# Performance work log

Hardware: AMD Instinct MI355X
Metric: run time of the kernel (lower is better)

## Reference

```python
import jax, jax.numpy as jnp
from jax import lax
import numpy as np

B, T, TW, EW = 32, 64, 32, 300   # dialogues, utterances, words, word-embed
H = 512                          # lstm hidden per direction
E = 2 * H                        # utterance embedding size
HH = 512                         # emotion hidden size
C = 7                            # output classes


def setup_inputs() -> dict:
    key = jax.random.key(0)
    ks = jax.random.split(key, 24)
    n = lambda k, shp: (jax.random.normal(k, shp, dtype=jnp.float32) * 0.05)
    inp = {
        "input_data": jax.random.normal(ks[0], (B, T, TW, EW), dtype=jnp.float32),
        # BiLSTM (torch gate order i,f,g,o)
        "lstm_Wih_f": n(ks[1], (4 * H, EW)), "lstm_Whh_f": n(ks[2], (4 * H, H)), "lstm_b_f": n(ks[3], (4 * H,)),
        "lstm_Wih_b": n(ks[4], (4 * H, EW)), "lstm_Whh_b": n(ks[5], (4 * H, H)), "lstm_b_b": n(ks[6], (4 * H,)),
        # attention weight
        "W_att": n(ks[7], (E, E)),
        # global-state GRUCell (torch gate order r,z,n)
        "g_Wih": n(ks[8], (3 * E, E)), "g_Whh": n(ks[9], (3 * E, E)), "g_bih": n(ks[10], (3 * E,)), "g_bhh": n(ks[11], (3 * E,)),
        # party-state GRUCell
        "p_Wih": n(ks[12], (3 * E, E)), "p_Whh": n(ks[13], (3 * E, E)), "p_bih": n(ks[14], (3 * E,)), "p_bhh": n(ks[15], (3 * E,)),
        # emotion-state GRUCell (input E, hidden HH)
        "e_Wih": n(ks[16], (3 * HH, E)), "e_Whh": n(ks[17], (3 * HH, HH)), "e_bih": n(ks[18], (3 * HH,)), "e_bhh": n(ks[19], (3 * HH,)),
        # classifier
        "cls_W": n(ks[20], (C, HH)), "cls_b": n(ks[21], (C,)),
    }
    return inp


def _gru_cell(x, h, Wih, Whh, bih, bhh):
    gi = x @ Wih.T + bih
    gh = h @ Whh.T + bhh
    ir, iz, inn = jnp.split(gi, 3, axis=-1)
    hr, hz, hn = jnp.split(gh, 3, axis=-1)
    r = jax.nn.sigmoid(ir + hr)
    z = jax.nn.sigmoid(iz + hz)
    n = jnp.tanh(inn + r * hn)
    return (1.0 - z) * n + z * h


def _lstm_last_hidden(xs, Wih, Whh, b):
    # xs: [Tw, N, Ew] -> final hidden [N, H]
    N = xs.shape[1]
    h0 = jnp.zeros((N, H), xs.dtype)

    def step(carry, x):
        h, c = carry
        g = x @ Wih.T + h @ Whh.T + b
        i_, f_, g_, o_ = jnp.split(g, 4, axis=-1)
        c2 = jax.nn.sigmoid(f_) * c + jax.nn.sigmoid(i_) * jnp.tanh(g_)
        h2 = jax.nn.sigmoid(o_) * jnp.tanh(c2)
        return (h2, c2), None

    (h, _), _ = lax.scan(step, (h0, h0), xs)
    return h


def _forward(input_data, lstm_Wih_f, lstm_Whh_f, lstm_b_f, lstm_Wih_b, lstm_Whh_b, lstm_b_b,
             W_att, g_Wih, g_Whh, g_bih, g_bhh, p_Wih, p_Whh, p_bih, p_bhh,
             e_Wih, e_Whh, e_bih, e_bhh, cls_W, cls_b):
    # ---- FeatureExtraction: BiLSTM over words, take fwd-last + bwd-first hidden ----
    x = input_data.reshape(B * T, TW, EW).transpose(1, 0, 2)          # [Tw, N, Ew]
    h_fwd = _lstm_last_hidden(x, lstm_Wih_f, lstm_Whh_f, lstm_b_f)     # [N, H]
    h_bwd = _lstm_last_hidden(x[::-1], lstm_Wih_b, lstm_Whh_b, lstm_b_b)  # [N, H]
    feats = jnp.concatenate([h_fwd, h_bwd], axis=-1).reshape(B, T, E)  # [B, T, 2H]

    # ---- EmotionDetection: sequential recurrence over utterances ----
    utt = feats.transpose(1, 0, 2)                                     # [T, B, E]
    hist0 = jnp.zeros((T + 1, B, E), feats.dtype)   # global_state history (idx 0 = zero init)
    party0 = jnp.zeros((2, B, E), feats.dtype)
    emo0 = jnp.zeros((B, HH), feats.dtype)
    l_idx = jnp.arange(T + 1)[:, None]              # [T+1, 1]

    def step(carry, inp):
        hist, party, emo = carry
        x_i, i = inp
        p = i % 2
        g_prev = hist[i]                                               # global_state[i]
        new_g = _gru_cell(x_i + party[p], g_prev, g_Wih, g_Whh, g_bih, g_bhh)
        hist = hist.at[i + 1].set(new_g)
        # attention over history indices 0..i (excludes the just-appended state)
        q = x_i @ W_att                                                # [B, E]
        scores = jnp.einsum('be,lbe->lb', q, hist)                     # [T+1, B]
        scores = jnp.where(l_idx <= i, scores, -jnp.inf)
        w = jax.nn.softmax(scores, axis=0)[:, :, None]                 # [T+1, B, 1]
        context = jnp.sum(hist * w, axis=0)                            # [B, E]
        new_p = _gru_cell(x_i + context, party[p], p_Wih, p_Whh, p_bih, p_bhh)
        party = party.at[p].set(new_p)
        emo = _gru_cell(new_p, emo, e_Wih, e_Whh, e_bih, e_bhh)        # [B, HH]
        return (hist, party, emo), emo

    _, emo_seq = lax.scan(step, (hist0, party0, emo0), (utt, jnp.arange(T)))
    emo_seq = emo_seq.transpose(1, 0, 2)                               # [B, T, HH]
    return emo_seq @ cls_W.T + cls_b                                   # [B, T, C]


def reference(input_data, lstm_Wih_f, lstm_Whh_f, lstm_b_f, lstm_Wih_b, lstm_Whh_b, lstm_b_b,
              W_att, g_Wih, g_Whh, g_bih, g_bhh, p_Wih, p_Whh, p_bih, p_bhh,
              e_Wih, e_Whh, e_bih, e_bhh, cls_W, cls_b):
    return _forward(input_data, lstm_Wih_f, lstm_Whh_f, lstm_b_f, lstm_Wih_b, lstm_Whh_b, lstm_b_b,
                    W_att, g_Wih, g_Whh, g_bih, g_bhh, p_Wih, p_Whh, p_bih, p_bhh,
                    e_Wih, e_Whh, e_bih, e_bhh, cls_W, cls_b)
```

## Files before the change

kernel.cpp:

```cpp
#include <hip/hip_runtime.h>
#include <math.h>

#define B_  32
#define T_  64
#define TW_ 32
#define EW_ 300
#define H_  512
#define E_  1024
#define HH_ 512
#define C_  7
#define N_  2048

typedef float f32x4 __attribute__((ext_vector_type(4)));
typedef short s16x8 __attribute__((ext_vector_type(8)));
typedef unsigned short u16;
typedef unsigned int u32;

__device__ __forceinline__ float sigm(float x){ return 1.f/(1.f+expf(-x)); }
__device__ __forceinline__ float bf2f(u16 u){
  union{float f; unsigned v;} x; x.v = ((unsigned)u)<<16; return x.f;
}
__device__ __forceinline__ u16 f2bf(float f){
  union{float f; unsigned v;} x; x.f = f;
  unsigned r = x.v + 0x7FFF + ((x.v>>16)&1);
  return (u16)(r>>16);
}
__device__ __forceinline__ void g2lds16(const void* g, void* l){
  __builtin_amdgcn_global_load_lds((const __attribute__((address_space(1))) u32*)g,
                                   (__attribute__((address_space(3))) u32*)l, 16, 0, 0);
}

__global__ __launch_bounds__(256) void k_pack_w(
    const float* __restrict__ Wih_f, const float* __restrict__ Whh_f,
    const float* __restrict__ Wih_b, const float* __restrict__ Whh_b,
    u16* __restrict__ Wpk2)
{
  size_t idx = (size_t)blockIdx.x*256 + threadIdx.x;
  if(idx >= (size_t)64*26*2048) return;
  int c   = (int)(idx & 31);
  int row = (int)((idx >> 5) & 63);
  int kc  = (int)((idx >> 11) % 26);
  int pan = (int)(idx / ((size_t)26*2048));
  int dir = pan >> 5, ms = pan & 31;
  int g = row >> 4, ml = row & 15;
  int R = g*512 + ms*16 + ml;
  int k = kc*32 + c;
  const float* Wih = dir ? Wih_b : Wih_f;
  const float* Whh = dir ? Whh_b : Whh_f;
  float v = (k < 320) ? ((k < EW_) ? Wih[(size_t)R*EW_ + k] : 0.f)
                      : Whh[(size_t)R*H_ + (k-320)];
  Wpk2[idx] = f2bf(v);
}

__global__ __launch_bounds__(256) void k_pack_x(
    const float* __restrict__ input, u16* __restrict__ xpk)
{
  size_t idx = (size_t)blockIdx.x*256 + threadIdx.x;
  if(idx >= (size_t)32*32*10*2048) return;
  int c   = (int)(idx & 31);
  int row = (int)((idx >> 5) & 63);
  int kc  = (int)((idx >> 11) % 10);
  int q2  = (int)((idx >> 11) / 10);
  int nt  = q2 & 31, wt = q2 >> 5;
  int n = nt*64 + row;
  int k = kc*32 + c;
  float v = (k < EW_) ? input[((size_t)n*TW_ + wt)*EW_ + k] : 0.f;
  xpk[idx] = f2bf(v);
}

__global__ __launch_bounds__(256) void k_f2bf(const float* __restrict__ src,
                                              u16* __restrict__ dst, int n)
{
  int idx = blockIdx.x*256 + threadIdx.x;
  if(idx < n) dst[idx] = f2bf(src[idx]);
}

__global__ __launch_bounds__(256) void k_wattT(const float* __restrict__ W,
                                               u16* __restrict__ dst)
{
  int idx = blockIdx.x*256 + threadIdx.x;
  if(idx >= E_*E_) return;
  int j = idx >> 10, k = idx & 1023;
  dst[idx] = f2bf(W[(size_t)k*E_ + j]);
}

__global__ __launch_bounds__(256, 6) void lstm6(
    const u16* __restrict__ xpk, const u16* __restrict__ Wpk2,
    const float* __restrict__ b_f, const float* __restrict__ b_b,
    const u16* __restrict__ hpk_in, u16* __restrict__ hpk_out,
    float* __restrict__ cpk, u16* __restrict__ featsbf, int t)
{
  const int pan = blockIdx.x, nt = blockIdx.y;
  const int dir = pan & 1, ms = pan >> 1;
  const int wt = dir ? (TW_-1-t) : t;
  const u16* srcW = Wpk2 + (size_t)(dir*32+ms)*26*2048;
  const u16* srcX = xpk + (size_t)(wt*32+nt)*10*2048;
  const u16* srcH = hpk_in + (size_t)(dir*32+nt)*16*2048;

  __shared__ __align__(16) u16 As[3][2048];
  __shared__ __align__(16) u16 Bs[3][2048];

  const int tid = threadIdx.x;
  const int w = tid >> 6, l = tid & 63;
  const int lr = l & 15, lh = l >> 4;

  f32x4 acc[4];
  #pragma unroll
  for(int g=0;g<4;g++) acc[g] = (f32x4){0.f,0.f,0.f,0.f};

  auto stage = [&](int kc, int b){
    const u16* aB = (kc < 10) ? (srcX + (size_t)kc*2048) : (srcH + (size_t)(kc-10)*2048);
    const u16* bB = srcW + (size_t)kc*2048;
    g2lds16((const char*)aB + w*1024 + l*16, (char*)&As[b][0] + w*1024);
    g2lds16((const char*)bB + w*1024 + l*16, (char*)&Bs[b][0] + w*1024);
  };

  stage(0, 0);
  stage(1, 1);
  #pragma unroll
  for(int kc=0; kc<26; ++kc){
    if(kc < 25) asm volatile("s_waitcnt vmcnt(2)" ::: "memory");
    else        asm volatile("s_waitcnt vmcnt(0)" ::: "memory");
    __builtin_amdgcn_s_barrier();
    __builtin_amdgcn_sched_barrier(0);
    if(kc+2 < 26) stage(kc+2, (kc+2)%3);
    const int cu = kc % 3;
    s16x8 av = *(const s16x8*)&As[cu][(w*16 + lr)*32 + lh*8];
    #pragma unroll
    for(int g=0; g<4; ++g){
      s16x8 bv = *(const s16x8*)&Bs[cu][(g*16 + lr)*32 + lh*8];
      acc[g] = __builtin_amdgcn_mfma_f32_16x16x32_bf16(av, bv, acc[g], 0,0,0);
    }
  }

  const float* bias = dir ? b_b : b_f;
  const int m = ms*16 + lr;
  const float bi = bias[m], bfv = bias[H_+m], bg = bias[2*H_+m], bo = bias[3*H_+m];
  float* cp = cpk + ((size_t)(dir*32+nt)*32 + ms)*1024;
  u16* hop = hpk_out + ((size_t)(dir*32+nt)*16 + (ms>>1))*2048 + (ms&1)*16;
  const int n0 = nt*64;
  #pragma unroll
  for(int r=0; r<4; ++r){
    const int row = w*16 + lh*4 + r;
    float gi = acc[0][r] + bi;
    float gf = acc[1][r] + bfv;
    float gc = acc[2][r] + bg;
    float go = acc[3][r] + bo;
    float c_old = cp[row*16 + lr];
    float c2 = sigm(gf)*c_old + sigm(gi)*tanhf(gc);
    float h2 = sigm(go)*tanhf(c2);
    cp[row*16 + lr] = c2;
    if(t == TW_-1) featsbf[(size_t)(n0+row)*E_ + dir*H_ + m] = f2bf(h2);
    else           hop[row*32 + lr] = f2bf(h2);
  }
}

__global__ __launch_bounds__(256) void k_qgemm(const u16* __restrict__ featsbf,
                                               const u16* __restrict__ WattT,
                                               float* __restrict__ q)
{
  const int n0 = blockIdx.x*64, j0 = blockIdx.y*64;
  __shared__ __align__(16) u16 As[64*40];
  __shared__ __align__(16) u16 Bs[64*40];
  const int tid = threadIdx.x;
  const int w = tid>>6, l = tid&63, lr = l&15, lk = (l>>4)*8;
  const int arow = tid>>2, ak8 = (tid&3)*8;

  f32x4 acc[4];
  #pragma unroll
  for(int i=0;i<4;i++) acc[i] = (f32x4){0.f,0.f,0.f,0.f};

  for(int kc=0; kc<32; ++kc){
    *(s16x8*)&As[arow*40 + ak8] = *(const s16x8*)&featsbf[(size_t)(n0+arow)*E_ + kc*32 + ak8];
    *(s16x8*)&Bs[arow*40 + ak8] = *(const s16x8*)&WattT[(size_t)(j0+arow)*E_ + kc*32 + ak8];
    __syncthreads();
    s16x8 av = *(const s16x8*)&As[(w*16 + lr)*40 + lk];
    #pragma unroll
    for(int mf=0; mf<4; ++mf){
      s16x8 bv = *(const s16x8*)&Bs[(mf*16 + lr)*40 + lk];
      acc[mf] = __builtin_amdgcn_mfma_f32_16x16x32_bf16(av, bv, acc[mf], 0,0,0);
    }
    __syncthreads();
  }
  #pragma unroll
  for(int mf=0; mf<4; ++mf)
    #pragma unroll
    for(int r=0; r<4; ++r){
      int n = n0 + w*16 + (l>>4)*4 + r;
      q[(size_t)n*E_ + j0 + mf*16 + lr] = acc[mf][r];
    }
}

struct GArg2 {
  const u16* xA; const u16* xB;
  long ldA; long ldB;
  const u16* W; int K;
};

__device__ __forceinline__ void gemm32v2(const GArg2 a, int R, int xt, int ks,
                                         int KS, int z, float* __restrict__ part,
                                         char* smem)
{
  u16* Xs0 = (u16*)smem;
  u16* Xs1 = Xs0 + 32*40;
  u16* Ws0 = Xs1 + 32*40;
  u16* Ws1 = Ws0 + 128*32;
  const int Kc = a.K / KS;
  const int nch = Kc >> 5;
  const int kb0 = ks * Kc;
  const int tid = threadIdx.x;
  const int w = tid>>6, l = tid&63, lr = l&15, lh = l>>4;

  f32x4 a00={0,0,0,0}, a01={0,0,0,0}, a10={0,0,0,0}, a11={0,0,0,0};

  auto issueW = [&](int c, u16* Wb){
    const int kb = kb0 + c*32;
    #pragma unroll
    for(int c2=0;c2<2;++c2){
      const int cc = w*2 + c2;
      const char* g = (const char*)(a.W + (size_t)(xt*128 + cc*16 + (l>>2))*a.K + kb) + (l&3)*16;
      g2lds16(g, (char*)Wb + cc*1024);
    }
  };
  auto loadX = [&](int c, short4* xr){
    const int kb = kb0 + c*32;
    const int row = tid>>3, k4 = (tid&7)*4;
    short4 xv = *(const short4*)&a.xA[(size_t)row*a.ldA + kb + k4];
    if(a.xB){
      short4 yv = *(const short4*)&a.xB[(size_t)row*a.ldB + kb + k4];
      xv.x = (short)f2bf(bf2f((u16)xv.x)+bf2f((u16)yv.x));
      xv.y = (short)f2bf(bf2f((u16)xv.y)+bf2f((u16)yv.y));
      xv.z = (short)f2bf(bf2f((u16)xv.z)+bf2f((u16)yv.z));
      xv.w = (short)f2bf(bf2f((u16)xv.w)+bf2f((u16)yv.w));
    }
    *xr = xv;
  };
  auto writeX = [&](short4 xv, u16* Xb){
    *(short4*)&Xb[(tid>>3)*40 + (tid&7)*4] = xv;
  };

  short4 xr;
  issueW(0, Ws0); loadX(0, &xr); writeX(xr, Xs0);
  __syncthreads();
  for(int c=0;c<nch;++c){
    u16* Xc = (c&1)?Xs1:Xs0; u16* Wc = (c&1)?Ws1:Ws0;
    u16* Xn = (c&1)?Xs0:Xs1; u16* Wn = (c&1)?Ws0:Ws1;
    const bool pre = (c+1 < nch);
    if(pre){ issueW(c+1, Wn); loadX(c+1, &xr); }
    s16x8 av0 = *(const s16x8*)&Xc[lr*40 + lh*8];
    s16x8 av1 = *(const s16x8*)&Xc[(16+lr)*40 + lh*8];
    s16x8 bv0 = *(const s16x8*)&Wc[(w*32 + lr)*32 + lh*8];
    s16x8 bv1 = *(const s16x8*)&Wc[(w*32 + 16 + lr)*32 + lh*8];
    a00 = __builtin_amdgcn_mfma_f32_16x16x32_bf16(av0, bv0, a00, 0,0,0);
    a01 = __builtin_amdgcn_mfma_f32_16x16x32_bf16(av0, bv1, a01, 0,0,0);
    a10 = __builtin_amdgcn_mfma_f32_16x16x32_bf16(av1, bv0, a10, 0,0,0);
    a11 = __builtin_amdgcn_mfma_f32_16x16x32_bf16(av1, bv1, a11, 0,0,0);
    if(pre) writeX(xr, Xn);
    __syncthreads();
  }
  float* dst = part + (size_t)((z*KS + ks)*B_)*R + xt*128 + w*32;
  f32x4 accs[2][2] = {{a00,a01},{a10,a11}};
  #pragma unroll
  for(int nf=0; nf<2; ++nf)
    #pragma unroll
    for(int mf=0; mf<2; ++mf)
      #pragma unroll
      for(int r=0; r<4; ++r){
        int n = nf*16 + lh*4 + r;
        dst[(size_t)n*R + mf*16 + lr] = accs[nf][mf][r];
      }
}

__device__ __forceinline__ void att_body(const float* __restrict__ q,
                                         const u16* __restrict__ histbf,
                                         const u16* __restrict__ featsbf,
                                         u16* __restrict__ xcbf,
                                         int i, int b, char* smem)
{
  float* qs = (float*)smem;
  float* sc = qs + E_;
  const int tid = threadIdx.x;
  *(float4*)&qs[tid*4] = *(const float4*)&q[((size_t)b*T_ + i)*E_ + tid*4];
  __syncthreads();
  const int wv = tid>>6, ln = tid&63;
  for(int L = wv; L <= i; L += 4){
    const u16* hl = histbf + ((size_t)L*B_ + b)*E_;
    float s = 0.f;
    s16x8 h0 = *(const s16x8*)&hl[ln*16];
    s16x8 h1 = *(const s16x8*)&hl[ln*16 + 8];
    #pragma unroll
    for(int j=0;j<8;j++){
      s += qs[ln*16 + j]     * bf2f((u16)h0[j]);
      s += qs[ln*16 + 8 + j] * bf2f((u16)h1[j]);
    }
    #pragma unroll
    for(int off=32; off; off>>=1) s += __shfl_down(s, off);
    if(ln == 0) sc[L] = s;
  }
  __syncthreads();
  if(tid < 64){
    float v  = (tid <= i) ? sc[tid] : -INFINITY;
    float mx = v;
    #pragma unroll
    for(int off=32; off; off>>=1) mx = fmaxf(mx, __shfl_xor(mx, off));
    float ex = (tid <= i) ? expf(v - mx) : 0.f;
    float sm = ex;
    #pragma unroll
    for(int off=32; off; off>>=1) sm += __shfl_xor(sm, off);
    sc[tid] = ex / sm;
  }
  __syncthreads();
  const int e4 = tid*4;
  float c0=0.f, c1=0.f, c2=0.f, c3=0.f;
  for(int L=0; L<=i; ++L){
    float wl = sc[L];
    short4 hv = *(const short4*)&histbf[((size_t)L*B_ + b)*E_ + e4];
    c0 += wl*bf2f((u16)hv.x);
    c1 += wl*bf2f((u16)hv.y);
    c2 += wl*bf2f((u16)hv.z);
    c3 += wl*bf2f((u16)hv.w);
  }
  const u16* xi = featsbf + ((size_t)b*T_ + i)*E_ + e4;
  xcbf[(size_t)b*E_ + e4 + 0] = f2bf(bf2f(xi[0]) + c0);
  xcbf[(size_t)b*E_ + e4 + 1] = f2bf(bf2f(xi[1]) + c1);
  xcbf[(size_t)b*E_ + e4 + 2] = f2bf(bf2f(xi[2]) + c2);
  xcbf[(size_t)b*E_ + e4 + 3] = f2bf(bf2f(xi[3]) + c3);
}

__device__ __forceinline__ void gru_comb(const float* __restrict__ part, int R, int J, int KS,
                                         const float* __restrict__ bih, const float* __restrict__ bhh,
                                         const float* __restrict__ hprev_f,
                                         float* __restrict__ dst_f,
                                         u16* __restrict__ dstbf,
                                         float* __restrict__ dst_seq, int idx)
{
  const int b = idx / J, e = idx - b*J;
  float ir=0.f, iz=0.f, in_=0.f, hr=0.f, hz=0.f, hn=0.f;
  for(int ks=0; ks<KS; ++ks){
    const float* p0 = part + (size_t)(ks*B_ + b)*R;
    const float* p1 = part + (size_t)((KS+ks)*B_ + b)*R;
    ir += p0[e]; iz += p0[J+e]; in_ += p0[2*J+e];
    hr += p1[e]; hz += p1[J+e]; hn  += p1[2*J+e];
  }
  ir += bih[e]; iz += bih[J+e]; in_ += bih[2*J+e];
  hr += bhh[e]; hz += bhh[J+e]; hn  += bhh[2*J+e];
  const float r = sigm(ir + hr);
  const float z = sigm(iz + hz);
  const float n = tanhf(in_ + r*hn);
  const float hp = hprev_f[(size_t)b*J + e];
  const float h2 = (1.f - z)*n + z*hp;
  dst_f[(size_t)b*J + e] = h2;
  dstbf[(size_t)b*J + e] = f2bf(h2);
  if(dst_seq) dst_seq[(size_t)b*J + e] = h2;
}

__global__ __launch_bounds__(256) void k_M(GArg2 g0, GArg2 g1,
    float* __restrict__ part_g,
    const float* __restrict__ q, const u16* __restrict__ histbf,
    const u16* __restrict__ featsbf, u16* __restrict__ xcbf,
    const float* __restrict__ part_p, const float* __restrict__ p_bih,
    const float* __restrict__ p_bhh, float* __restrict__ partyf_pm1,
    u16* __restrict__ partybf_pm1,
    const float* __restrict__ part_e, const float* __restrict__ e_bih,
    const float* __restrict__ e_bhh, float* __restrict__ emof,
    u16* __restrict__ emobf, float* __restrict__ emo_seq, int i)
{
  __shared__ __align__(16) char smem[21504];
  const int x = blockIdx.x;
  if(x < 384){
    if(i >= T_) return;
    const int xt = x % 24, ks = (x/24) & 7, z = x/192;
    gemm32v2(z ? g1 : g0, 3*E_, xt, ks, 8, z, part_g, smem);
  } else if(x < 416){
    if(i >= T_) return;
    att_body(q, histbf, featsbf, xcbf, i, x-384, smem);
  } else if(x < 544){
    const int ip = i-1;
    if(ip < 0 || ip >= T_) return;
    gru_comb(part_p, 3*E_, E_, 8, p_bih, p_bhh, partyf_pm1, partyf_pm1,
             partybf_pm1, nullptr, (x-416)*256 + (int)threadIdx.x);
  } else {
    const int ie = i-2;
    if(ie < 0 || ie >= T_) return;
    gru_comb(part_e, 3*HH_, HH_, 8, e_bih, e_bhh, emof, emof, emobf,
             emo_seq + (size_t)ie*B_*HH_, (x-544)*256 + (int)threadIdx.x);
  }
}

__global__ __launch_bounds__(256) void k_B2(GArg2 p0, GArg2 p1, GArg2 e0, GArg2 e1,
    const float* __restrict__ part_g,
    const float* __restrict__ g_bih, const float* __restrict__ g_bhh,
    const float* __restrict__ gf_prev, float* __restrict__ gf_next,
    u16* __restrict__ histbf,
    float* __restrict__ part_p, float* __restrict__ part_e, int i)
{
  __shared__ __align__(16) char smem[21504];
  const int x = blockIdx.x;
  if(x < 128){
    if(i >= T_) return;
    gru_comb(part_g, 3*E_, E_, 8, g_bih, g_bhh, gf_prev, gf_next,
             histbf + (size_t)(i+1)*B_*E_, nullptr, x*256 + (int)threadIdx.x);
  } else if(x < 512){
    if(i >= T_) return;
    const int ix = x-128, xt = ix % 24, ks = (ix/24) & 7, z = ix/192;
    gemm32v2(z ? p1 : p0, 3*E_, xt, ks, 8, z, part_p, smem);
  } else {
    if(i < 1) return;
    const int ix = x-512, xt = ix % 12, ks = (ix/12) & 7, z = ix/96;
    gemm32v2(z ? e1 : e0, 3*HH_, xt, ks, 8, z, part_e, smem);
  }
}

__global__ __launch_bounds__(256) void classify(const float* __restrict__ emo_seq,
    const float* __restrict__ clsW, const float* __restrict__ clsb, float* __restrict__ out)
{
  const int idx = blockIdx.x*256 + threadIdx.x;
  if(idx >= B_*T_*C_) return;
  const int c = idx % C_;
  const int bt = idx / C_;
  const int t = bt % T_, b = bt / T_;
  const float* e = emo_seq + (size_t)(t*B_ + b)*HH_;
  const float* w = clsW + (size_t)c*HH_;
  float s = clsb[c];
  for(int h=0; h<HH_; ++h) s += e[h]*w[h];
  out[idx] = s;
}

extern "C" void kernel_launch(void* const* d_in, const int* in_sizes, int n_in,
                              void* d_out, int out_size, void* d_ws, size_t ws_size,
                              hipStream_t stream)
{
  const float* input  = (const float*)d_in[0];
  const float* Wih_f  = (const float*)d_in[1];
  const float* Whh_f  = (const float*)d_in[2];
  const float* b_f    = (const float*)d_in[3];
  const float* Wih_b  = (const float*)d_in[4];
  const float* Whh_b  = (const float*)d_in[5];
  const float* b_b    = (const float*)d_in[6];
  const float* W_att  = (const float*)d_in[7];
  const float* g_Wih  = (const float*)d_in[8];
  const float* g_Whh  = (const float*)d_in[9];
  const float* g_bih  = (const float*)d_in[10];
  const float* g_bhh  = (const float*)d_in[11];
  const float* p_Wih  = (const float*)d_in[12];
  const float* p_Whh  = (const float*)d_in[13];
  const float* p_bih  = (const float*)d_in[14];
  const float* p_bhh  = (const float*)d_in[15];
  const float* e_Wih  = (const float*)d_in[16];
  const float* e_Whh  = (const float*)d_in[17];
  const float* e_bih  = (const float*)d_in[18];
  const float* e_bhh  = (const float*)d_in[19];
  const float* cls_W  = (const float*)d_in[20];
  const float* cls_b  = (const float*)d_in[21];

  char* base = (char*)d_ws;
  size_t off = 0;
  auto alloc = [&](size_t bytes)->char*{
    char* p = base + off; off += (bytes + 255) & ~(size_t)255; return p;
  };
  u16*   Wpk2    = (u16*)alloc((size_t)64*26*2048*2);
  u16*   xpk     = (u16*)alloc((size_t)32*32*10*2048*2);
  u16*   hpkA    = (u16*)alloc((size_t)2*32*16*2048*2);
  u16*   hpkB    = (u16*)alloc((size_t)2*32*16*2048*2);
  float* cpk     = (float*)alloc((size_t)2*32*32*1024*4);
  u16*   featsbf = (u16*)alloc((size_t)N_*E_*2);
  u16*   eWih    = (u16*)alloc((size_t)3*HH_*E_*2);
  u16*   eWhh    = (u16*)alloc((size_t)3*HH_*HH_*2);
  u16*   histbf  = (u16*)alloc((size_t)(T_+1)*B_*E_*2);
  float* gfbuf   = (float*)alloc((size_t)2*B_*E_*4);
  float* partyf  = (float*)alloc((size_t)2*B_*E_*4);
  u16*   partybf = (u16*)alloc((size_t)2*B_*E_*2);
  float* emof    = (float*)alloc((size_t)B_*HH_*4);
  u16*   emobf   = (u16*)alloc((size_t)B_*HH_*2);
  float* emo_seq = (float*)alloc((size_t)T_*B_*HH_*4);
  u16*   xcbf    = (u16*)alloc((size_t)B_*E_*2);
  float* part_p  = (float*)alloc((size_t)16*B_*3*E_*4);
  u16*   gWih    = (u16*)((char*)xpk + 0);
  u16*   gWhh    = (u16*)((char*)xpk + 6291456);
  u16*   pWih    = (u16*)((char*)xpk + 12582912);
  u16*   pWhh    = (u16*)((char*)xpk + 18874368);
  float* part_e  = (float*)((char*)xpk + 25165824);
  float* q       = (float*)((char*)xpk + 28311552);
  u16*   WattT   = (u16*)((char*)xpk + 36700160);
  float* part_g  = (float*)hpkA;

  hipMemsetAsync(hpkA,    0, (size_t)2*32*16*2048*2, stream);
  hipMemsetAsync(cpk,     0, (size_t)2*32*32*1024*4, stream);
  hipMemsetAsync(histbf,  0, (size_t)B_*E_*2, stream);
  hipMemsetAsync(gfbuf,   0, (size_t)B_*E_*4, stream);
  hipMemsetAsync(partyf,  0, (size_t)2*B_*E_*4, stream);
  hipMemsetAsync(partybf, 0, (size_t)2*B_*E_*2, stream);
  hipMemsetAsync(emof,    0, (size_t)B_*HH_*4, stream);
  hipMemsetAsync(emobf,   0, (size_t)B_*HH_*2, stream);

  k_pack_w<<<dim3(((size_t)64*26*2048 + 255)/256), 256, 0, stream>>>(Wih_f, Whh_f, Wih_b, Whh_b, Wpk2);
  k_pack_x<<<dim3(((size_t)32*32*10*2048 + 255)/256), 256, 0, stream>>>(input, xpk);

  for(int t=0; t<TW_; ++t){
    u16* hin  = (t & 1) ? hpkB : hpkA;
    u16* hout = (t & 1) ? hpkA : hpkB;
    lstm6<<<dim3(64, 32), 256, 0, stream>>>(xpk, Wpk2, b_f, b_b, hin, hout, cpk, featsbf, t);
  }

  k_f2bf<<<dim3((3*E_*E_+255)/256), 256, 0, stream>>>(g_Wih, gWih, 3*E_*E_);
  k_f2bf<<<dim3((3*E_*E_+255)/256), 256, 0, stream>>>(g_Whh, gWhh, 3*E_*E_);
  k_f2bf<<<dim3((3*E_*E_+255)/256), 256, 0, stream>>>(p_Wih, pWih, 3*E_*E_);
  k_f2bf<<<dim3((3*E_*E_+255)/256), 256, 0, stream>>>(p_Whh, pWhh, 3*E_*E_);
  k_f2bf<<<dim3((3*HH_*E_+255)/256), 256, 0, stream>>>(e_Wih, eWih, 3*HH_*E_);
  k_f2bf<<<dim3((3*HH_*HH_+255)/256), 256, 0, stream>>>(e_Whh, eWhh, 3*HH_*HH_);
  k_wattT<<<dim3((E_*E_+255)/256), 256, 0, stream>>>(W_att, WattT);

  k_qgemm<<<dim3(32, 16), 256, 0, stream>>>(featsbf, WattT, q);

  for(int i=0; i<=T_+1; ++i){
    GArg2 ga0{ featsbf + (size_t)i*E_, partybf + (size_t)(i&1)*B_*E_, (long)T_*E_, (long)E_, gWih, E_ };
    GArg2 ga1{ histbf + (size_t)i*B_*E_, nullptr, (long)E_, 0, gWhh, E_ };
    k_M<<<dim3(608), 256, 0, stream>>>(ga0, ga1, part_g, q, histbf, featsbf, xcbf,
                                       part_p, p_bih, p_bhh,
                                       partyf + (size_t)((i-1)&1)*B_*E_,
                                       partybf + (size_t)((i-1)&1)*B_*E_,
                                       part_e, e_bih, e_bhh, emof, emobf, emo_seq, i);
    if(i <= T_){
      GArg2 pa0{ xcbf, nullptr, (long)E_, 0, pWih, E_ };
      GArg2 pa1{ partybf + (size_t)(i&1)*B_*E_, nullptr, (long)E_, 0, pWhh, E_ };
      GArg2 ea0{ partybf + (size_t)((i-1)&1)*B_*E_, nullptr, (long)E_, 0, eWih, E_ };
      GArg2 ea1{ emobf, nullptr, (long)HH_, 0, eWhh, HH_ };
      k_B2<<<dim3(704), 256, 0, stream>>>(pa0, pa1, ea0, ea1, part_g,
                                          g_bih, g_bhh,
                                          gfbuf + (size_t)(i&1)*B_*E_,
                                          gfbuf + (size_t)((i+1)&1)*B_*E_,
                                          histbf, part_p, part_e, i);
    }
  }

  classify<<<dim3((B_*T_*C_+255)/256), 256, 0, stream>>>(emo_seq, cls_W, cls_b, (float*)d_out);
}
```

Measured before the change: 2.444 ms.

## Double-buffer LSTM step kernel and issue all GRU GEMM loads upfront

The LSTM step kernel drops from a triple-buffered to a double-buffered LDS ring and adds a second barrier per chunk, which shrinks shared memory so more blocks can be resident (launch bound raised to 8 waves). The split-K GRU GEMM helper becomes a templated version that issues every K-chunk's weight and input loads at once into a larger LDS area, waits once, then runs all the MFMAs. This removes the per-chunk barriers and serialized load latency. The cost is doubled shared memory in the fused step kernels, which may lower occupancy, and an extra barrier inside the LSTM loop.

```diff
diff --git a/kernel.cpp b/kernel.cpp
--- a/kernel.cpp
+++ b/kernel.cpp
@@ -84,7 +84,7 @@
   dst[idx] = f2bf(W[(size_t)k*E_ + j]);
 }
 
-__global__ __launch_bounds__(256, 6) void lstm6(
+__global__ __launch_bounds__(256, 8) void lstm7(
     const u16* __restrict__ xpk, const u16* __restrict__ Wpk2,
     const float* __restrict__ b_f, const float* __restrict__ b_b,
     const u16* __restrict__ hpk_in, u16* __restrict__ hpk_out,
@@ -97,8 +97,8 @@
   const u16* srcX = xpk + (size_t)(wt*32+nt)*10*2048;
   const u16* srcH = hpk_in + (size_t)(dir*32+nt)*16*2048;
 
-  __shared__ __align__(16) u16 As[3][2048];
-  __shared__ __align__(16) u16 Bs[3][2048];
+  __shared__ __align__(16) u16 As[2][2048];
+  __shared__ __align__(16) u16 Bs[2][2048];
 
   const int tid = threadIdx.x;
   const int w = tid >> 6, l = tid & 63;
@@ -116,21 +116,21 @@
   };
 
   stage(0, 0);
-  stage(1, 1);
   #pragma unroll
   for(int kc=0; kc<26; ++kc){
+    if(kc+1 < 26) stage(kc+1, (kc+1)&1);
     if(kc < 25) asm volatile("s_waitcnt vmcnt(2)" ::: "memory");
     else        asm volatile("s_waitcnt vmcnt(0)" ::: "memory");
     __builtin_amdgcn_s_barrier();
     __builtin_amdgcn_sched_barrier(0);
-    if(kc+2 < 26) stage(kc+2, (kc+2)%3);
-    const int cu = kc % 3;
+    const int cu = kc & 1;
     s16x8 av = *(const s16x8*)&As[cu][(w*16 + lr)*32 + lh*8];
     #pragma unroll
     for(int g=0; g<4; ++g){
       s16x8 bv = *(const s16x8*)&Bs[cu][(g*16 + lr)*32 + lh*8];
       acc[g] = __builtin_amdgcn_mfma_f32_16x16x32_bf16(av, bv, acc[g], 0,0,0);
     }
+    if(kc < 25) __builtin_amdgcn_s_barrier();
   }
 
   const float* bias = dir ? b_b : b_f;
@@ -197,34 +197,33 @@
   const u16* W; int K;
 };
 
-__device__ __forceinline__ void gemm32v2(const GArg2 a, int R, int xt, int ks,
+template<int NCH>
+__device__ __forceinline__ void gemm32v3(const GArg2 a, int R, int xt, int ks,
                                          int KS, int z, float* __restrict__ part,
                                          char* smem)
 {
-  u16* Xs0 = (u16*)smem;
-  u16* Xs1 = Xs0 + 32*40;
-  u16* Ws0 = Xs1 + 32*40;
-  u16* Ws1 = Ws0 + 128*32;
+  u16* Xs = (u16*)smem;
+  u16* Ws = (u16*)smem + 4*1280;
   const int Kc = a.K / KS;
-  const int nch = Kc >> 5;
   const int kb0 = ks * Kc;
   const int tid = threadIdx.x;
   const int w = tid>>6, l = tid&63, lr = l&15, lh = l>>4;
 
-  f32x4 a00={0,0,0,0}, a01={0,0,0,0}, a10={0,0,0,0}, a11={0,0,0,0};
-
-  auto issueW = [&](int c, u16* Wb){
+  #pragma unroll
+  for(int c=0;c<NCH;++c){
     const int kb = kb0 + c*32;
     #pragma unroll
     for(int c2=0;c2<2;++c2){
       const int cc = w*2 + c2;
       const char* g = (const char*)(a.W + (size_t)(xt*128 + cc*16 + (l>>2))*a.K + kb) + (l&3)*16;
-      g2lds16(g, (char*)Wb + cc*1024);
-    }
-  };
-  auto loadX = [&](int c, short4* xr){
+      g2lds16(g, (char*)(Ws + c*4096) + cc*1024);
+    }
+  }
+  const int row = tid>>3, k4 = (tid&7)*4;
+  short4 xr[NCH];
+  #pragma unroll
+  for(int c=0;c<NCH;++c){
     const int kb = kb0 + c*32;
-    const int row = tid>>3, k4 = (tid&7)*4;
     short4 xv = *(const short4*)&a.xA[(size_t)row*a.ldA + kb + k4];
     if(a.xB){
       short4 yv = *(const short4*)&a.xB[(size_t)row*a.ldB + kb + k4];
@@ -233,20 +232,21 @@
       xv.z = (short)f2bf(bf2f((u16)xv.z)+bf2f((u16)yv.z));
       xv.w = (short)f2bf(bf2f((u16)xv.w)+bf2f((u16)yv.w));
     }
-    *xr = xv;
-  };
-  auto writeX = [&](short4 xv, u16* Xb){
-    *(short4*)&Xb[(tid>>3)*40 + (tid&7)*4] = xv;
-  };
-
-  short4 xr;
-  issueW(0, Ws0); loadX(0, &xr); writeX(xr, Xs0);
-  __syncthreads();
-  for(int c=0;c<nch;++c){
-    u16* Xc = (c&1)?Xs1:Xs0; u16* Wc = (c&1)?Ws1:Ws0;
-    u16* Xn = (c&1)?Xs0:Xs1; u16* Wn = (c&1)?Ws0:Ws1;
-    const bool pre = (c+1 < nch);
-    if(pre){ issueW(c+1, Wn); loadX(c+1, &xr); }
+    xr[c] = xv;
+  }
+  #pragma unroll
+  for(int c=0;c<NCH;++c)
+    *(short4*)&Xs[c*1280 + row*40 + k4] = xr[c];
+
+  asm volatile("s_waitcnt vmcnt(0) lgkmcnt(0)" ::: "memory");
+  __builtin_amdgcn_s_barrier();
+  __builtin_amdgcn_sched_barrier(0);
+
+  f32x4 a00={0,0,0,0}, a01={0,0,0,0}, a10={0,0,0,0}, a11={0,0,0,0};
+  #pragma unroll
+  for(int c=0;c<NCH;++c){
+    const u16* Xc = Xs + c*1280;
+    const u16* Wc = Ws + c*4096;
     s16x8 av0 = *(const s16x8*)&Xc[lr*40 + lh*8];
     s16x8 av1 = *(const s16x8*)&Xc[(16+lr)*40 + lh*8];
     s16x8 bv0 = *(const s16x8*)&Wc[(w*32 + lr)*32 + lh*8];
@@ -255,8 +255,6 @@
     a01 = __builtin_amdgcn_mfma_f32_16x16x32_bf16(av0, bv1, a01, 0,0,0);
     a10 = __builtin_amdgcn_mfma_f32_16x16x32_bf16(av1, bv0, a10, 0,0,0);
     a11 = __builtin_amdgcn_mfma_f32_16x16x32_bf16(av1, bv1, a11, 0,0,0);
-    if(pre) writeX(xr, Xn);
-    __syncthreads();
   }
   float* dst = part + (size_t)((z*KS + ks)*B_)*R + xt*128 + w*32;
   f32x4 accs[2][2] = {{a00,a01},{a10,a11}};
@@ -365,12 +363,12 @@
     const float* __restrict__ e_bhh, float* __restrict__ emof,
     u16* __restrict__ emobf, float* __restrict__ emo_seq, int i)
 {
-  __shared__ __align__(16) char smem[21504];
+  __shared__ __align__(16) char smem[43008];
   const int x = blockIdx.x;
   if(x < 384){
     if(i >= T_) return;
     const int xt = x % 24, ks = (x/24) & 7, z = x/192;
-    gemm32v2(z ? g1 : g0, 3*E_, xt, ks, 8, z, part_g, smem);
+    gemm32v3<4>(z ? g1 : g0, 3*E_, xt, ks, 8, z, part_g, smem);
   } else if(x < 416){
     if(i >= T_) return;
     att_body(q, histbf, featsbf, xcbf, i, x-384, smem);
@@ -394,7 +392,7 @@
     u16* __restrict__ histbf,
     float* __restrict__ part_p, float* __restrict__ part_e, int i)
 {
-  __shared__ __align__(16) char smem[21504];
+  __shared__ __align__(16) char smem[43008];
   const int x = blockIdx.x;
   if(x < 128){
     if(i >= T_) return;
@@ -403,11 +401,12 @@
   } else if(x < 512){
     if(i >= T_) return;
     const int ix = x-128, xt = ix % 24, ks = (ix/24) & 7, z = ix/192;
-    gemm32v2(z ? p1 : p0, 3*E_, xt, ks, 8, z, part_p, smem);
+    gemm32v3<4>(z ? p1 : p0, 3*E_, xt, ks, 8, z, part_p, smem);
   } else {
     if(i < 1) return;
     const int ix = x-512, xt = ix % 12, ks = (ix/12) & 7, z = ix/96;
-    gemm32v2(z ? e1 : e0, 3*HH_, xt, ks, 8, z, part_e, smem);
+    if(z) gemm32v3<2>(e1, 3*HH_, xt, ks, 8, 1, part_e, smem);
+    else  gemm32v3<4>(e0, 3*HH_, xt, ks, 8, 0, part_e, smem);
   }
 }
 
@@ -499,7 +498,7 @@
   for(int t=0; t<TW_; ++t){
     u16* hin  = (t & 1) ? hpkB : hpkA;
     u16* hout = (t & 1) ? hpkA : hpkB;
-    lstm6<<<dim3(64, 32), 256, 0, stream>>>(xpk, Wpk2, b_f, b_b, hin, hout, cpk, featsbf, t);
+    lstm7<<<dim3(64, 32), 256, 0, stream>>>(xpk, Wpk2, b_f, b_b, hin, hout, cpk, featsbf, t);
   }
 
   k_f2bf<<<dim3((3*E_*E_+255)/256), 256, 0, stream>>>(g_Wih, gWih, 3*E_*E_);
```

New measurement: 2.357 ms. -3.6%, faster.
